# Performance work log

Measured on AMD Instinct MI355X. Metric: run time of the kernel, lower is better.

Reference implementation:

```python
import jax, jax.numpy as jnp
import numpy as np

IN_CH, OUT_CH, K = 4096, 4096, 64
C, F = IN_CH // K, OUT_CH // K  # 64, 64
BS = 256


def setup_inputs() -> dict:
    key = jax.random.key(0)
    k1, k2 = jax.random.split(key)
    x = jax.random.normal(k1, (BS, IN_CH), dtype=jnp.float32)
    stdv = 1.0 / float(np.sqrt(C))  # matches torch init: uniform(-1/sqrt(in_channels), ...)
    weights = jax.random.uniform(k2, (F, C, K), dtype=jnp.float32, minval=-stdv, maxval=stdv)
    return {"x": x, "weights": weights}


def reference(x, weights):
    # Faithful, batched version of Linear_BC_func.forward:
    #   per sample: ifft(fft(w, 'ortho') * fft(x, 'backward'), 'ortho').real, summed over C.
    # The per-sample Python loop and the C-sum are fused: sum over C is done in the
    # frequency domain (linearity of ifft), and the batch is handled by one einsum.
    bs = x.shape[0]
    f, c, k = weights.shape
    xk = x.reshape(bs, c, k)
    Wf = jnp.fft.fft(weights, norm="ortho")      # (F, C, K) complex64
    Xf = jnp.fft.fft(xk, norm="backward")        # (BS, C, K) complex64
    Sf = jnp.einsum("fck,bck->bfk", Wf, Xf)      # sum over C in frequency domain
    out = jnp.fft.ifft(Sf, norm="ortho").real.astype(jnp.float32)  # torch .float() keeps real part
    return out.reshape(bs, f * k)
```

## Files before the change

kernel.cpp:

```cpp
#include <hip/hip_runtime.h>


#define KDIM 4096

typedef __attribute__((ext_vector_type(8)))  short s16x8;
typedef __attribute__((ext_vector_type(4)))  float f32x4;
typedef __attribute__((ext_vector_type(16))) float f32x16;
typedef unsigned short u16;

__device__ __forceinline__ u16 f2bf(float f) {
  unsigned int u = __float_as_uint(f);
  u += 0x7FFF + ((u >> 16) & 1);
  return (u16)(u >> 16);
}

__global__ __launch_bounds__(256) void pack_kernel(const float* __restrict__ x,
                                                   u16* __restrict__ Xp) {
  __shared__ __align__(16) u16 tile[32 * 264];
  const int tid = threadIdx.x;
  const int rg  = blockIdx.x >> 4;
  const int cg  = blockIdx.x & 15;

  #pragma unroll
  for (int i = 0; i < 4; ++i) {
    int g    = i * 2048 + tid * 8;
    int row  = g >> 8;
    int kloc = g & 255;
    const float4* src = (const float4*)(x + (size_t)(rg * 32 + row) * 4096 + cg * 256 + kloc);
    float4 v0 = src[0], v1 = src[1];
    union { u16 u[8]; uint4 v; } o;
    o.u[0] = f2bf(v0.x); o.u[1] = f2bf(v0.y); o.u[2] = f2bf(v0.z); o.u[3] = f2bf(v0.w);
    o.u[4] = f2bf(v1.x); o.u[5] = f2bf(v1.y); o.u[6] = f2bf(v1.z); o.u[7] = f2bf(v1.w);
    *(uint4*)(tile + row * 264 + kloc) = o.v;
  }
  __syncthreads();

  const int lane = tid & 63;
  const int fw   = tid >> 6;
  #pragma unroll
  for (int i = 0; i < 4; ++i) {
    int fidx = i * 4 + fw;
    int cl   = fidx >> 2;
    int kk   = fidx & 3;
    int c    = cg * 4 + cl;
    uint4 v = *(const uint4*)(tile + (lane & 31) * 264 + cl * 64 + kk * 16 + (lane >> 5) * 8);
    size_t u = ((size_t)((c * 8 + rg) * 4 + kk) << 6) + lane;
    *(uint4*)(Xp + (u << 3)) = v;
  }
}

__global__ __launch_bounds__(1024, 4) void gemm_f2(const u16* __restrict__ Xp,
                                                   const float* __restrict__ w,
                                                   float* __restrict__ out) {
  extern __shared__ __align__(16) char pool[];
  u16*   tab = (u16*)pool;
  float* red = (float*)pool;

  const int tid   = threadIdx.x;
  const int lane  = tid & 63;
  const int wid   = tid >> 6;
  const int cg    = wid & 1;
  const int kg    = wid >> 1;
  const int l31   = lane & 31;
  const int lh    = lane >> 5;
  const int q     = blockIdx.x & 7;
  const int fg    = blockIdx.x >> 3;

  #pragma unroll
  for (int j = 0; j < 8; ++j) {
    int t    = wid * 8 + j;
    int fidx = t >> 6;
    int c    = t & 63;
    u16 bv = f2bf(w[((size_t)(fg * 2 + fidx) << 12) + (c << 6) + lane]);
    u16* T = tab + t * 576;
    #pragma unroll
    for (int m = 0; m < 8; ++m) {
      int i = (-(lane + m)) & 63;
      T[m * 72 + i] = bv;
    }
  }

  int bofs0, bofs1, bofs2, bofs3;
  {
    int i0;
    i0 = (lh * 8 - l31)      & 63; bofs0 = (i0 & 7) * 71 + i0;
    i0 = (lh * 8 - l31 - 16) & 63; bofs1 = (i0 & 7) * 71 + i0;
    i0 = (lh * 8 - l31 - 32) & 63; bofs2 = (i0 & 7) * 71 + i0;
    i0 = (lh * 8 - l31 - 48) & 63; bofs3 = (i0 & 7) * 71 + i0;
  }

  const u16* abase = Xp + ((size_t)kg * 8 * 16384 + q * 2048 + lane * 8);
  const u16* tabf  = tab + cg * 36864;

  s16x8 A0_0, A0_1, A0_2, A0_3;
  s16x8 A1_0, A1_1, A1_2, A1_3;
  s16x8 A2_0, A2_1, A2_2, A2_3;

  #define ALOAD(SET, T)                                                   \
    { const u16* nb_ = abase + (size_t)(T) * 16384;                       \
      asm volatile("global_load_dwordx4 %0, %4, off\n\t"                  \
                   "global_load_dwordx4 %1, %4, off offset:1024\n\t"      \
                   "global_load_dwordx4 %2, %4, off offset:2048\n\t"      \
                   "global_load_dwordx4 %3, %4, off offset:3072"          \
                   : "=&v"(A##SET##_0), "=&v"(A##SET##_1),                \
                     "=&v"(A##SET##_2), "=&v"(A##SET##_3)                 \
                   : "v"(nb_)); }

  #define WAITV_(N) asm volatile("s_waitcnt vmcnt(" #N ")")
  #define WAITV(N)  WAITV_(N)

  f32x16 acc0 = {}, acc1 = {};

  __syncthreads();

  ALOAD(0, 0)
  ALOAD(1, 1)

  #define STEP(T, CUR, PRE, DOPRE, WN)                                        \
    {                                                                         \
      if (DOPRE) ALOAD(PRE, (T) + 2)                                          \
      const u16* Tb = tabf + (kg * 8 + (T)) * 576;                            \
      s16x8 b0 = *(const s16x8*)(Tb + bofs0);                                 \
      s16x8 b1 = *(const s16x8*)(Tb + bofs1);                                 \
      s16x8 b2 = *(const s16x8*)(Tb + bofs2);                                 \
      s16x8 b3 = *(const s16x8*)(Tb + bofs3);                                 \
      WAITV(WN);                                                              \
      __builtin_amdgcn_sched_barrier(0);                                      \
      acc0 = __builtin_amdgcn_mfma_f32_32x32x16_bf16(A##CUR##_0, b0, acc0, 0, 0, 0); \
      acc1 = __builtin_amdgcn_mfma_f32_32x32x16_bf16(A##CUR##_0, b2, acc1, 0, 0, 0); \
      acc0 = __builtin_amdgcn_mfma_f32_32x32x16_bf16(A##CUR##_1, b3, acc0, 0, 0, 0); \
      acc1 = __builtin_amdgcn_mfma_f32_32x32x16_bf16(A##CUR##_1, b1, acc1, 0, 0, 0); \
      acc0 = __builtin_amdgcn_mfma_f32_32x32x16_bf16(A##CUR##_2, b2, acc0, 0, 0, 0); \
      acc1 = __builtin_amdgcn_mfma_f32_32x32x16_bf16(A##CUR##_2, b0, acc1, 0, 0, 0); \
      acc0 = __builtin_amdgcn_mfma_f32_32x32x16_bf16(A##CUR##_3, b1, acc0, 0, 0, 0); \
      acc1 = __builtin_amdgcn_mfma_f32_32x32x16_bf16(A##CUR##_3, b3, acc1, 0, 0, 0); \
    }

  STEP(0, 0, 2, 1, 8)
  STEP(1, 1, 0, 1, 8)
  STEP(2, 2, 1, 1, 8)
  STEP(3, 0, 2, 1, 8)
  STEP(4, 1, 0, 1, 8)
  STEP(5, 2, 1, 1, 8)
  STEP(6, 0, 2, 0, 4)
  STEP(7, 1, 2, 0, 0)

  __syncthreads();
  {
    float* slot = red + (cg * 8 + kg) * 2048;
    #pragma unroll
    for (int i = 0; i < 4; ++i) {
      f32x4 v0 = {acc0[4*i], acc0[4*i+1], acc0[4*i+2], acc0[4*i+3]};
      f32x4 v1 = {acc1[4*i], acc1[4*i+1], acc1[4*i+2], acc1[4*i+3]};
      *(f32x4*)(slot + ((i)     * 64 + lane) * 4) = v0;
      *(f32x4*)(slot + ((i + 4) * 64 + lane) * 4) = v1;
    }
  }
  __syncthreads();
  {
    const int rcg = tid >> 9;
    const int ii  = (tid >> 6) & 7;
    const int sl  = tid & 63;
    f32x4 s = {};
    #pragma unroll
    for (int k = 0; k < 8; ++k)
      s += *(const f32x4*)(red + (size_t)(rcg * 8 + k) * 2048 + (ii * 64 + sl) * 4);
    const int col  = ((fg * 2 + rcg) << 6) + (ii >> 2) * 32 + (sl & 31);
    const int rowb = q * 32 + 8 * (ii & 3) + 4 * (sl >> 5);
    #pragma unroll
    for (int e = 0; e < 4; ++e)
      out[(size_t)(rowb + e) * 4096 + col] = s[e];
  }
}

extern "C" void kernel_launch(void* const* d_in, const int* in_sizes, int n_in,
                              void* d_out, int out_size, void* d_ws, size_t ws_size,
                              hipStream_t stream) {
  const float* x = (const float*)d_in[0];
  const float* w = (const float*)d_in[1];
  float* out = (float*)d_out;

  u16* Xp = (u16*)d_ws;

  pack_kernel<<<128, 256, 0, stream>>>(x, Xp);
  gemm_f2<<<256, 1024, 147456, stream>>>(Xp, w, out);
}
```

Before: 19.74 us.

## Fuse bf16 packing of x into the GEMM kernel, dropping the pack pass

Removes the separate pack kernel that converted x to bf16 and rearranged it in workspace. The GEMM now loads fp32 x rows directly and converts them to bf16 in registers before the MFMA, saving one launch and a workspace round trip. The hand-written asm prefetch pipeline with explicit waitcnt is replaced by a plain unrolled loop left to the compiler to schedule. Each x element is now read as fp32 (twice the bytes) by every F-group block, so global traffic per block rises.

```diff
diff --git a/kernel.cpp b/kernel.cpp
--- a/kernel.cpp
+++ b/kernel.cpp
@@ -1,4 +1,5 @@
 #include <hip/hip_runtime.h>
+#include <hip/hip_bf16.h>
 
 
 #define KDIM 4096
@@ -14,44 +15,18 @@
   return (u16)(u >> 16);
 }
 
-__global__ __launch_bounds__(256) void pack_kernel(const float* __restrict__ x,
-                                                   u16* __restrict__ Xp) {
-  __shared__ __align__(16) u16 tile[32 * 264];
-  const int tid = threadIdx.x;
-  const int rg  = blockIdx.x >> 4;
-  const int cg  = blockIdx.x & 15;
-
-  #pragma unroll
-  for (int i = 0; i < 4; ++i) {
-    int g    = i * 2048 + tid * 8;
-    int row  = g >> 8;
-    int kloc = g & 255;
-    const float4* src = (const float4*)(x + (size_t)(rg * 32 + row) * 4096 + cg * 256 + kloc);
-    float4 v0 = src[0], v1 = src[1];
-    union { u16 u[8]; uint4 v; } o;
-    o.u[0] = f2bf(v0.x); o.u[1] = f2bf(v0.y); o.u[2] = f2bf(v0.z); o.u[3] = f2bf(v0.w);
-    o.u[4] = f2bf(v1.x); o.u[5] = f2bf(v1.y); o.u[6] = f2bf(v1.z); o.u[7] = f2bf(v1.w);
-    *(uint4*)(tile + row * 264 + kloc) = o.v;
-  }
-  __syncthreads();
-
-  const int lane = tid & 63;
-  const int fw   = tid >> 6;
-  #pragma unroll
-  for (int i = 0; i < 4; ++i) {
-    int fidx = i * 4 + fw;
-    int cl   = fidx >> 2;
-    int kk   = fidx & 3;
-    int c    = cg * 4 + cl;
-    uint4 v = *(const uint4*)(tile + (lane & 31) * 264 + cl * 64 + kk * 16 + (lane >> 5) * 8);
-    size_t u = ((size_t)((c * 8 + rg) * 4 + kk) << 6) + lane;
-    *(uint4*)(Xp + (u << 3)) = v;
-  }
+__device__ __forceinline__ s16x8 cvt8(float4 lo, float4 hi) {
+  union { __hip_bfloat162 h[4]; s16x8 v; } u;
+  u.h[0] = __float22bfloat162_rn(make_float2(lo.x, lo.y));
+  u.h[1] = __float22bfloat162_rn(make_float2(lo.z, lo.w));
+  u.h[2] = __float22bfloat162_rn(make_float2(hi.x, hi.y));
+  u.h[3] = __float22bfloat162_rn(make_float2(hi.z, hi.w));
+  return u.v;
 }
 
-__global__ __launch_bounds__(1024, 4) void gemm_f2(const u16* __restrict__ Xp,
-                                                   const float* __restrict__ w,
-                                                   float* __restrict__ out) {
+__global__ __launch_bounds__(1024, 4) void gemm_fused(const float* __restrict__ x,
+                                                      const float* __restrict__ w,
+                                                      float* __restrict__ out) {
   extern __shared__ __align__(16) char pool[];
   u16*   tab = (u16*)pool;
   float* red = (float*)pool;
@@ -89,61 +64,34 @@
     i0 = (lh * 8 - l31 - 48) & 63; bofs3 = (i0 & 7) * 71 + i0;
   }
 
-  const u16* abase = Xp + ((size_t)kg * 8 * 16384 + q * 2048 + lane * 8);
-  const u16* tabf  = tab + cg * 36864;
-
-  s16x8 A0_0, A0_1, A0_2, A0_3;
-  s16x8 A1_0, A1_1, A1_2, A1_3;
-  s16x8 A2_0, A2_1, A2_2, A2_3;
-
-  #define ALOAD(SET, T)                                                   \
-    { const u16* nb_ = abase + (size_t)(T) * 16384;                       \
-      asm volatile("global_load_dwordx4 %0, %4, off\n\t"                  \
-                   "global_load_dwordx4 %1, %4, off offset:1024\n\t"      \
-                   "global_load_dwordx4 %2, %4, off offset:2048\n\t"      \
-                   "global_load_dwordx4 %3, %4, off offset:3072"          \
-                   : "=&v"(A##SET##_0), "=&v"(A##SET##_1),                \
-                     "=&v"(A##SET##_2), "=&v"(A##SET##_3)                 \
-                   : "v"(nb_)); }
-
-  #define WAITV_(N) asm volatile("s_waitcnt vmcnt(" #N ")")
-  #define WAITV(N)  WAITV_(N)
+  const float* xrow = x + ((size_t)(q * 32 + l31) << 12) + lh * 8;
+  const u16*   tabf = tab + cg * 36864;
 
   f32x16 acc0 = {}, acc1 = {};
 
   __syncthreads();
 
-  ALOAD(0, 0)
-  ALOAD(1, 1)
-
-  #define STEP(T, CUR, PRE, DOPRE, WN)                                        \
-    {                                                                         \
-      if (DOPRE) ALOAD(PRE, (T) + 2)                                          \
-      const u16* Tb = tabf + (kg * 8 + (T)) * 576;                            \
-      s16x8 b0 = *(const s16x8*)(Tb + bofs0);                                 \
-      s16x8 b1 = *(const s16x8*)(Tb + bofs1);                                 \
-      s16x8 b2 = *(const s16x8*)(Tb + bofs2);                                 \
-      s16x8 b3 = *(const s16x8*)(Tb + bofs3);                                 \
-      WAITV(WN);                                                              \
-      __builtin_amdgcn_sched_barrier(0);                                      \
-      acc0 = __builtin_amdgcn_mfma_f32_32x32x16_bf16(A##CUR##_0, b0, acc0, 0, 0, 0); \
-      acc1 = __builtin_amdgcn_mfma_f32_32x32x16_bf16(A##CUR##_0, b2, acc1, 0, 0, 0); \
-      acc0 = __builtin_amdgcn_mfma_f32_32x32x16_bf16(A##CUR##_1, b3, acc0, 0, 0, 0); \
-      acc1 = __builtin_amdgcn_mfma_f32_32x32x16_bf16(A##CUR##_1, b1, acc1, 0, 0, 0); \
-      acc0 = __builtin_amdgcn_mfma_f32_32x32x16_bf16(A##CUR##_2, b2, acc0, 0, 0, 0); \
-      acc1 = __builtin_amdgcn_mfma_f32_32x32x16_bf16(A##CUR##_2, b0, acc1, 0, 0, 0); \
-      acc0 = __builtin_amdgcn_mfma_f32_32x32x16_bf16(A##CUR##_3, b1, acc0, 0, 0, 0); \
-      acc1 = __builtin_amdgcn_mfma_f32_32x32x16_bf16(A##CUR##_3, b3, acc1, 0, 0, 0); \
-    }
-
-  STEP(0, 0, 2, 1, 8)
-  STEP(1, 1, 0, 1, 8)
-  STEP(2, 2, 1, 1, 8)
-  STEP(3, 0, 2, 1, 8)
-  STEP(4, 1, 0, 1, 8)
-  STEP(5, 2, 1, 1, 8)
-  STEP(6, 0, 2, 0, 4)
-  STEP(7, 1, 2, 0, 0)
+  #pragma unroll
+  for (int T = 0; T < 8; ++T) {
+    const float* xs = xrow + ((kg * 8 + T) << 6);
+    s16x8 a0 = cvt8(*(const float4*)(xs +  0), *(const float4*)(xs +  4));
+    s16x8 a1 = cvt8(*(const float4*)(xs + 16), *(const float4*)(xs + 20));
+    s16x8 a2 = cvt8(*(const float4*)(xs + 32), *(const float4*)(xs + 36));
+    s16x8 a3 = cvt8(*(const float4*)(xs + 48), *(const float4*)(xs + 52));
+    const u16* Tb = tabf + (kg * 8 + T) * 576;
+    s16x8 b0 = *(const s16x8*)(Tb + bofs0);
+    s16x8 b1 = *(const s16x8*)(Tb + bofs1);
+    s16x8 b2 = *(const s16x8*)(Tb + bofs2);
+    s16x8 b3 = *(const s16x8*)(Tb + bofs3);
+    acc0 = __builtin_amdgcn_mfma_f32_32x32x16_bf16(a0, b0, acc0, 0, 0, 0);
+    acc1 = __builtin_amdgcn_mfma_f32_32x32x16_bf16(a0, b2, acc1, 0, 0, 0);
+    acc0 = __builtin_amdgcn_mfma_f32_32x32x16_bf16(a1, b3, acc0, 0, 0, 0);
+    acc1 = __builtin_amdgcn_mfma_f32_32x32x16_bf16(a1, b1, acc1, 0, 0, 0);
+    acc0 = __builtin_amdgcn_mfma_f32_32x32x16_bf16(a2, b2, acc0, 0, 0, 0);
+    acc1 = __builtin_amdgcn_mfma_f32_32x32x16_bf16(a2, b0, acc1, 0, 0, 0);
+    acc0 = __builtin_amdgcn_mfma_f32_32x32x16_bf16(a3, b1, acc0, 0, 0, 0);
+    acc1 = __builtin_amdgcn_mfma_f32_32x32x16_bf16(a3, b3, acc1, 0, 0, 0);
+  }
 
   __syncthreads();
   {
@@ -180,8 +128,5 @@
   const float* w = (const float*)d_in[1];
   float* out = (float*)d_out;
 
-  u16* Xp = (u16*)d_ws;
-
-  pack_kernel<<<128, 256, 0, stream>>>(x, Xp);
-  gemm_f2<<<256, 1024, 147456, stream>>>(Xp, w, out);
+  gemm_fused<<<256, 1024, 147456, stream>>>(x, w, out);
 }
```

Result: slower. 37.90 us (+91.9%).
